# Performance work log

Hardware: AMD Instinct MI355X
Metric: run time of the kernel (lower is better)

## Reference

```python
import jax, jax.numpy as jnp
import numpy as np

IN_FEATURES = 512
OUT_FEATURES = 512
GRID_MIN = -2.0
GRID_MAX = 2.0
NUM_GRIDS = 8
SPLINE_SCALE = 0.1
BATCH = 16384


def setup_inputs() -> dict:
    key = jax.random.key(0)
    kx, kw = jax.random.split(key)
    x = jax.random.normal(kx, (BATCH, IN_FEATURES), dtype=jnp.float32)
    grid = jnp.linspace(GRID_MIN, GRID_MAX, NUM_GRIDS, dtype=jnp.float32)
    spline_weight = (
        jax.random.normal(kw, (IN_FEATURES * NUM_GRIDS, OUT_FEATURES), dtype=jnp.float32)
        * SPLINE_SCALE
    )
    return {"x": x, "grid": grid, "spline_weight": spline_weight}


def reference(x, grid, spline_weight):
    # denominator h = (grid_max - grid_min) / (num_grids - 1)
    h = (GRID_MAX - GRID_MIN) / (NUM_GRIDS - 1)
    # basis: [B, in_features, num_grids]
    basis = jnp.exp(-jnp.square((x[..., None] - grid) / h))
    # flatten to [B, in_features * num_grids] and GEMM
    return basis.reshape(basis.shape[0], -1) @ spline_weight
```

## Files before the change

### kernel.cpp

```cpp
#include <hip/hip_runtime.h>
#include <hip/hip_bf16.h>

#define BATCH 16384
#define IN_F 512
#define OUT_F 512
#define NG 8
#define KTOT (IN_F * NG)

#define SH    2.1019642153762872f
#define SSTEP 1.2011224087864498f
#define BC0N  4.2039284307525745f
#define RC1   2.4022448175728996f

typedef __attribute__((ext_vector_type(8))) short short8;
typedef __attribute__((ext_vector_type(4))) float f32x4;
typedef __attribute__((ext_vector_type(2))) float f32x2;
typedef __attribute__((ext_vector_type(4))) unsigned int u32x4;
typedef __attribute__((ext_vector_type(2))) unsigned int u32x2;

__device__ __forceinline__ unsigned fbits(float f) {
    union { float f; unsigned u; } v; v.f = f; return v.u;
}
__device__ __forceinline__ unsigned pack2bf(float lo, float hi) {
    return __builtin_amdgcn_perm(fbits(hi) + 0x8000u, fbits(lo) + 0x8000u,
                                 0x07060302u);
}

__device__ __forceinline__ void lds_barrier() {
    __asm__ volatile("" ::: "memory");
    __builtin_amdgcn_sched_barrier(0);
    __builtin_amdgcn_s_waitcnt(0xC07F);
    __builtin_amdgcn_s_barrier();
    __builtin_amdgcn_sched_barrier(0);
    __asm__ volatile("" ::: "memory");
}

__global__ void wt_swizzle(const float* __restrict__ W, unsigned short* __restrict__ Wt) {
    const int gid  = blockIdx.x * 256 + threadIdx.x;
    const int lane = gid & 63;
    const int f    = (gid >> 6) & 7;
    const int kt   = (gid >> 9) & 63;
    const int s    = gid >> 15;
    const int j  = f & 3, kk = f >> 2;
    const int l15 = lane & 15, lq = lane >> 4;
    const int n  = s * 64 + j * 16 + l15;
    const int k0 = kt * 64 + kk * 32 + lq * 8;
    constexpr float QS[8] = {1.0f,
                             3.6787944117144233e-1f,
                             1.8315638888734179e-2f,
                             1.2340980408667956e-4f,
                             1.1253517471925912e-7f,
                             1.3887943864964021e-11f,
                             2.3195228302435693e-16f,
                             5.2428856633634640e-22f};
    u32x4 pk;
#pragma unroll
    for (int e = 0; e < 4; ++e)
        pk[e] = pack2bf(W[(size_t)(k0 + 2 * e) * OUT_F + n] * QS[2 * e],
                        W[(size_t)(k0 + 2 * e + 1) * OUT_F + n] * QS[2 * e + 1]);
    *(u32x4*)(Wt + (size_t)gid * 8) = pk;
}

__global__ __launch_bounds__(512, 2) void gauss_gemm18(
        const float* __restrict__ X, const unsigned short* __restrict__ Wt,
        float* __restrict__ Out) {
    __shared__ __align__(16) unsigned short sA[8 * 8192];

    const int tid  = threadIdx.x;
    const int lane = tid & 63;
    const int wave = tid >> 6;
    const int wm   = wave >> 2;
    const int wn   = wave & 3;
    const int nb = (blockIdx.x & 7) * 32 + (blockIdx.x >> 3);
    const int cb = nb >> 7;
    const int rb = nb & 127;
    const int m0 = rb * 128;
    const int l15 = lane & 15;
    const int lq  = lane >> 4;
    const int s   = cb * 4 + wn;

    const int arow = tid & 127;
    const int fp   = tid >> 7;
    const int aw0 = arow * 64 + (((2 * fp)     ^ (arow & 7)) << 3);
    const int aw1 = arow * 64 + (((2 * fp + 1) ^ (arow & 7)) << 3);
    const float* xlp = X + (size_t)(m0 + arow) * IN_F + fp * 2;

    int aofs[2][4];
#pragma unroll
    for (int kk = 0; kk < 2; ++kk)
#pragma unroll
        for (int i = 0; i < 4; ++i)
            aofs[kk][i] = (wm * 64 + i * 16 + l15) * 64 +
                          (((kk * 4 + lq) ^ (l15 & 7)) << 3);

    const unsigned short* bptr = Wt + (size_t)s * 262144 + lane * 8;

    f32x4 acc[4][4];
#pragma unroll
    for (int i = 0; i < 4; ++i)
#pragma unroll
        for (int j = 0; j < 4; ++j)
            acc[i][j] = (f32x4){0.f, 0.f, 0.f, 0.f};

    auto stageA = [&](f32x2 xv, int slot) {
        unsigned short* base = sA + slot * 8192;
#pragma unroll
        for (int h = 0; h < 2; ++h) {
            const float t0  = fmaf(h ? xv.y : xv.x, SH, BC0N);
            const float rho = __builtin_amdgcn_exp2f(t0 * RC1);
            const float v0  = __builtin_amdgcn_exp2f(-t0 * t0);
            const float r2  = rho * rho;
            const float v1 = v0 * rho;
            const float v2 = v0 * r2, v3 = v1 * r2;
            const float v4 = v2 * r2, v5 = v3 * r2;
            const float v6 = v4 * r2, v7 = v5 * r2;
            union { __hip_bfloat162 hh[4]; u32x4 u; } pk;
            pk.hh[0] = __float22bfloat162_rn(make_float2(v0, v1));
            pk.hh[1] = __float22bfloat162_rn(make_float2(v2, v3));
            pk.hh[2] = __float22bfloat162_rn(make_float2(v4, v5));
            pk.hh[3] = __float22bfloat162_rn(make_float2(v6, v7));
            *(u32x4*)(base + (h ? aw1 : aw0)) = pk.u;
        }
    };

    short8 bfA[8], bfB[8];
    f32x2 xu, xv;

    {
        f32x2 x0 = *(const f32x2*)(xlp);
        f32x2 x1 = *(const f32x2*)(xlp + 8);
        f32x2 x2 = *(const f32x2*)(xlp + 16);
        f32x2 x3 = *(const f32x2*)(xlp + 24);
        xu = *(const f32x2*)(xlp + 32);
        xv = *(const f32x2*)(xlp + 40);
#pragma unroll
        for (int f = 0; f < 8; ++f)
            bfA[f] = *(const short8*)(bptr + f * 512);
        stageA(x0, 0);
        stageA(x1, 1);
        stageA(x2, 2);
        stageA(x3, 3);
        lds_barrier();
    }

#define GG18(KT0, S, BU, BF, XUSE)                                             \
    {                                                                          \
        const int kt  = (KT0) + (S);                                           \
        const int kn1 = (kt + 1 < 64) ? kt + 1 : 63;                           \
        const int kn6 = (kt + 6 < 64) ? kt + 6 : 63;                           \
        _Pragma("unroll")                                                      \
        for (int f = 0; f < 8; ++f)                                            \
            BF[f] = *(const short8*)(bptr + (size_t)kn1 * 4096 + f * 512);     \
        short8 af[2][4];                                                       \
        _Pragma("unroll")                                                      \
        for (int kk = 0; kk < 2; ++kk)                                         \
            _Pragma("unroll")                                                  \
            for (int i = 0; i < 4; ++i)                                        \
                af[kk][i] = *(const short8*)(sA + (S) * 8192 + aofs[kk][i]);   \
        stageA(XUSE, ((S) + 4) & 7);                                           \
        XUSE = *(const f32x2*)(xlp + (size_t)kn6 * 8);                         \
        __builtin_amdgcn_s_setprio(1);                                         \
        _Pragma("unroll")                                                      \
        for (int kk = 0; kk < 2; ++kk)                                         \
            _Pragma("unroll")                                                  \
            for (int i = 0; i < 4; ++i)                                        \
                _Pragma("unroll")                                              \
                for (int j = 0; j < 4; ++j)                                    \
                    acc[i][j] = __builtin_amdgcn_mfma_f32_16x16x32_bf16(       \
                        af[kk][i], BU[kk * 4 + j], acc[i][j], 0, 0, 0);        \
        __builtin_amdgcn_s_setprio(0);                                         \
        if (((S) & 3) == 3) lds_barrier();                                     \
    }

    for (int kt0 = 0; kt0 < 64; kt0 += 8) {
        GG18(kt0, 0, bfA, bfB, xu)
        GG18(kt0, 1, bfB, bfA, xv)
        GG18(kt0, 2, bfA, bfB, xu)
        GG18(kt0, 3, bfB, bfA, xv)
        GG18(kt0, 4, bfA, bfB, xu)
        GG18(kt0, 5, bfB, bfA, xv)
        GG18(kt0, 6, bfA, bfB, xu)
        GG18(kt0, 7, bfB, bfA, xv)
    }
#undef GG18

#pragma unroll
    for (int i = 0; i < 4; ++i) {
        const int r0 = m0 + wm * 64 + i * 16 + lq * 4;
#pragma unroll
        for (int j = 0; j < 4; ++j) {
            const int c = cb * 256 + wn * 64 + j * 16 + l15;
#pragma unroll
            for (int e = 0; e < 4; ++e)
                Out[(size_t)(r0 + e) * OUT_F + c] = acc[i][j][e];
        }
    }
}

#define BM 128
#define BN 128
#define BK 64
#define LDA 72
#define LDB 72

__global__ __launch_bounds__(256, 2) void gauss_gemm_fb(
        const float* __restrict__ X, const float* __restrict__ W,
        float* __restrict__ Out) {
    __shared__ __align__(16) unsigned short sA[BM * LDA];
    __shared__ __align__(16) unsigned short sB2[BN * LDB];

    const int tid  = threadIdx.x;
    const int lane = tid & 63;
    const int wave = tid >> 6;
    const int rb = blockIdx.x >> 2;
    const int cbx = blockIdx.x & 3;
    const int m0 = rb * BM;
    const int n0 = cbx * BN;
    const int wr = (wave >> 1) * 64;
    const int wc = (wave & 1) * 64;
    const int l15 = lane & 15;
    const int lq  = lane >> 4;

    f32x4 acc[4][4];
#pragma unroll
    for (int i = 0; i < 4; ++i)
#pragma unroll
        for (int j = 0; j < 4; ++j)
            acc[i][j] = (f32x4){0.f, 0.f, 0.f, 0.f};

    const int arow = tid & 127;
    const int axq  = tid >> 7;

    for (int kt = 0; kt < KTOT / BK; ++kt) {
        const int k0  = kt * BK;
        const int xc0 = kt * (BK / NG);

        const f32x4 xv = *(const f32x4*)(X + (size_t)(m0 + arow) * IN_F + xc0 + 4 * axq);
        unsigned short* sArow = sA + arow * LDA + axq * 32;
#pragma unroll
        for (int j = 0; j < 4; ++j) {
            const float xs = xv[j] * SH;
            u32x4 pk;
#pragma unroll
            for (int g = 0; g < 8; g += 2) {
                float t0 = xs + (BC0N - g * SSTEP);
                float t1 = xs + (BC0N - (g + 1) * SSTEP);
                pk[g >> 1] = pack2bf(__builtin_amdgcn_exp2f(-t0 * t0),
                                     __builtin_amdgcn_exp2f(-t1 * t1));
            }
            *(u32x4*)(sArow + j * 8) = pk;
        }

#pragma unroll
        for (int p = 0; p < 8; ++p) {
            int id = p * 256 + tid;
            int n  = id & 127;
            int k4 = id >> 7;
            const float* wp = W + (size_t)(k0 + k4 * 4) * OUT_F + n0 + n;
            u32x2 v;
            v[0] = pack2bf(wp[0], wp[OUT_F]);
            v[1] = pack2bf(wp[2 * OUT_F], wp[3 * OUT_F]);
            *(u32x2*)(sB2 + n * LDB + k4 * 4) = v;
        }

        __syncthreads();

#pragma unroll
        for (int kk = 0; kk < BK; kk += 32) {
            short8 af[4], bfv[4];
#pragma unroll
            for (int i = 0; i < 4; ++i)
                af[i] = *(const short8*)(sA + (wr + i * 16 + l15) * LDA + kk + lq * 8);
#pragma unroll
            for (int i = 0; i < 4; ++i)
                bfv[i] = *(const short8*)(sB2 + (wc + i * 16 + l15) * LDB + kk + lq * 8);
#pragma unroll
            for (int i = 0; i < 4; ++i)
#pragma unroll
                for (int j = 0; j < 4; ++j)
                    acc[i][j] = __builtin_amdgcn_mfma_f32_16x16x32_bf16(af[i], bfv[j], acc[i][j], 0, 0, 0);
        }

        __syncthreads();
    }

#pragma unroll
    for (int i = 0; i < 4; ++i) {
        const int r0 = m0 + wr + i * 16 + lq * 4;
#pragma unroll
        for (int j = 0; j < 4; ++j) {
            const int c = n0 + wc + j * 16 + l15;
#pragma unroll
            for (int e = 0; e < 4; ++e)
                Out[(size_t)(r0 + e) * OUT_F + c] = acc[i][j][e];
        }
    }
}

extern "C" void kernel_launch(void* const* d_in, const int* in_sizes, int n_in,
                              void* d_out, int out_size, void* d_ws, size_t ws_size,
                              hipStream_t stream) {
    (void)in_sizes; (void)n_in; (void)out_size;
    const float* X = (const float*)d_in[0];
    const float* W = (const float*)d_in[2];
    float* Out = (float*)d_out;

    const size_t wt_bytes = (size_t)KTOT * OUT_F * sizeof(unsigned short);
    if (ws_size >= wt_bytes) {
        unsigned short* Wt = (unsigned short*)d_ws;
        wt_swizzle<<<dim3(KTOT * OUT_F / 8 / 256), 256, 0, stream>>>(W, Wt);
        gauss_gemm18<<<dim3((BATCH / 128) * (OUT_F / 256)), 512, 0, stream>>>(X, Wt, Out);
    } else {
        gauss_gemm_fb<<<dim3((BATCH / BM) * (OUT_F / BN)), 256, 0, stream>>>(X, W, Out);
    }
}
```

Before: 154.7 us.

## Split waves into producer (basis compute) and consumer (MFMA) roles

```diff
diff --git a/kernel.cpp b/kernel.cpp
--- a/kernel.cpp
+++ b/kernel.cpp
@@ -61,93 +61,50 @@
     *(u32x4*)(Wt + (size_t)gid * 8) = pk;
 }
 
-__global__ __launch_bounds__(512, 2) void gauss_gemm18(
+__global__ __launch_bounds__(512, 2) void gauss_gemm20(
         const float* __restrict__ X, const unsigned short* __restrict__ Wt,
         float* __restrict__ Out) {
-    __shared__ __align__(16) unsigned short sA[8 * 8192];
+    __shared__ __align__(16) unsigned short sA[8 * 4096];
 
     const int tid  = threadIdx.x;
     const int lane = tid & 63;
     const int wave = tid >> 6;
-    const int wm   = wave >> 2;
-    const int wn   = wave & 3;
-    const int nb = (blockIdx.x & 7) * 32 + (blockIdx.x >> 3);
-    const int cb = nb >> 7;
-    const int rb = nb & 127;
-    const int m0 = rb * 128;
+    const int nb = (blockIdx.x & 7) * 64 + (blockIdx.x >> 3);
+    const int cb = nb >> 8;
+    const int rb = nb & 255;
+    const int m0 = rb * 64;
     const int l15 = lane & 15;
     const int lq  = lane >> 4;
-    const int s   = cb * 4 + wn;
-
-    const int arow = tid & 127;
-    const int fp   = tid >> 7;
-    const int aw0 = arow * 64 + (((2 * fp)     ^ (arow & 7)) << 3);
-    const int aw1 = arow * 64 + (((2 * fp + 1) ^ (arow & 7)) << 3);
-    const float* xlp = X + (size_t)(m0 + arow) * IN_F + fp * 2;
-
-    int aofs[2][4];
-#pragma unroll
-    for (int kk = 0; kk < 2; ++kk)
+
+    if (wave < 4) {
+        const int s = cb * 4 + wave;
+        const unsigned short* bptr = Wt + (size_t)s * 262144 + lane * 8;
+
+        int aofs[2][4];
+#pragma unroll
+        for (int kk = 0; kk < 2; ++kk)
+#pragma unroll
+            for (int i = 0; i < 4; ++i)
+                aofs[kk][i] = (i * 16 + l15) * 64 +
+                              (((kk * 4 + lq) ^ (l15 & 7)) << 3);
+
+        f32x4 acc[4][4];
 #pragma unroll
         for (int i = 0; i < 4; ++i)
-            aofs[kk][i] = (wm * 64 + i * 16 + l15) * 64 +
-                          (((kk * 4 + lq) ^ (l15 & 7)) << 3);
-
-    const unsigned short* bptr = Wt + (size_t)s * 262144 + lane * 8;
-
-    f32x4 acc[4][4];
-#pragma unroll
-    for (int i = 0; i < 4; ++i)
-#pragma unroll
-        for (int j = 0; j < 4; ++j)
-            acc[i][j] = (f32x4){0.f, 0.f, 0.f, 0.f};
-
-    auto stageA = [&](f32x2 xv, int slot) {
-        unsigned short* base = sA + slot * 8192;
-#pragma unroll
-        for (int h = 0; h < 2; ++h) {
-            const float t0  = fmaf(h ? xv.y : xv.x, SH, BC0N);
-            const float rho = __builtin_amdgcn_exp2f(t0 * RC1);
-            const float v0  = __builtin_amdgcn_exp2f(-t0 * t0);
-            const float r2  = rho * rho;
-            const float v1 = v0 * rho;
-            const float v2 = v0 * r2, v3 = v1 * r2;
-            const float v4 = v2 * r2, v5 = v3 * r2;
-            const float v6 = v4 * r2, v7 = v5 * r2;
-            union { __hip_bfloat162 hh[4]; u32x4 u; } pk;
-            pk.hh[0] = __float22bfloat162_rn(make_float2(v0, v1));
-            pk.hh[1] = __float22bfloat162_rn(make_float2(v2, v3));
-            pk.hh[2] = __float22bfloat162_rn(make_float2(v4, v5));
-            pk.hh[3] = __float22bfloat162_rn(make_float2(v6, v7));
-            *(u32x4*)(base + (h ? aw1 : aw0)) = pk.u;
-        }
-    };
-
-    short8 bfA[8], bfB[8];
-    f32x2 xu, xv;
-
-    {
-        f32x2 x0 = *(const f32x2*)(xlp);
-        f32x2 x1 = *(const f32x2*)(xlp + 8);
-        f32x2 x2 = *(const f32x2*)(xlp + 16);
-        f32x2 x3 = *(const f32x2*)(xlp + 24);
-        xu = *(const f32x2*)(xlp + 32);
-        xv = *(const f32x2*)(xlp + 40);
+#pragma unroll
+            for (int j = 0; j < 4; ++j)
+                acc[i][j] = (f32x4){0.f, 0.f, 0.f, 0.f};
+
+        short8 bfA[8], bfB[8];
 #pragma unroll
         for (int f = 0; f < 8; ++f)
             bfA[f] = *(const short8*)(bptr + f * 512);
-        stageA(x0, 0);
-        stageA(x1, 1);
-        stageA(x2, 2);
-        stageA(x3, 3);
+
         lds_barrier();
-    }
-
-#define GG18(KT0, S, BU, BF, XUSE)                                             \
+
+#define CONS20(KT, BU, BF)                                                     \
     {                                                                          \
-        const int kt  = (KT0) + (S);                                           \
-        const int kn1 = (kt + 1 < 64) ? kt + 1 : 63;                           \
-        const int kn6 = (kt + 6 < 64) ? kt + 6 : 63;                           \
+        const int kn1 = ((KT) + 1 < 64) ? (KT) + 1 : 63;                       \
         _Pragma("unroll")                                                      \
         for (int f = 0; f < 8; ++f)                                            \
             BF[f] = *(const short8*)(bptr + (size_t)kn1 * 4096 + f * 512);     \
@@ -156,9 +113,8 @@
         for (int kk = 0; kk < 2; ++kk)                                         \
             _Pragma("unroll")                                                  \
             for (int i = 0; i < 4; ++i)                                        \
-                af[kk][i] = *(const short8*)(sA + (S) * 8192 + aofs[kk][i]);   \
-        stageA(XUSE, ((S) + 4) & 7);                                           \
-        XUSE = *(const f32x2*)(xlp + (size_t)kn6 * 8);                         \
+                af[kk][i] = *(const short8*)(sA + ((KT) & 7) * 4096 +          \
+                                             aofs[kk][i]);                     \
         __builtin_amdgcn_s_setprio(1);                                         \
         _Pragma("unroll")                                                      \
         for (int kk = 0; kk < 2; ++kk)                                         \
@@ -169,30 +125,112 @@
                     acc[i][j] = __builtin_amdgcn_mfma_f32_16x16x32_bf16(       \
                         af[kk][i], BU[kk * 4 + j], acc[i][j], 0, 0, 0);        \
         __builtin_amdgcn_s_setprio(0);                                         \
-        if (((S) & 3) == 3) lds_barrier();                                     \
-    }
-
-    for (int kt0 = 0; kt0 < 64; kt0 += 8) {
-        GG18(kt0, 0, bfA, bfB, xu)
-        GG18(kt0, 1, bfB, bfA, xv)
-        GG18(kt0, 2, bfA, bfB, xu)
-        GG18(kt0, 3, bfB, bfA, xv)
-        GG18(kt0, 4, bfA, bfB, xu)
-        GG18(kt0, 5, bfB, bfA, xv)
-        GG18(kt0, 6, bfA, bfB, xu)
-        GG18(kt0, 7, bfB, bfA, xv)
-    }
-#undef GG18
-
-#pragma unroll
-    for (int i = 0; i < 4; ++i) {
-        const int r0 = m0 + wm * 64 + i * 16 + lq * 4;
-#pragma unroll
-        for (int j = 0; j < 4; ++j) {
-            const int c = cb * 256 + wn * 64 + j * 16 + l15;
-#pragma unroll
-            for (int e = 0; e < 4; ++e)
-                Out[(size_t)(r0 + e) * OUT_F + c] = acc[i][j][e];
+    }
+
+        for (int kt0 = 0; kt0 < 64; kt0 += 8) {
+            CONS20(kt0 + 0, bfA, bfB)
+            CONS20(kt0 + 1, bfB, bfA)
+            CONS20(kt0 + 2, bfA, bfB)
+            CONS20(kt0 + 3, bfB, bfA)
+            lds_barrier();
+            CONS20(kt0 + 4, bfA, bfB)
+            CONS20(kt0 + 5, bfB, bfA)
+            CONS20(kt0 + 6, bfA, bfB)
+            CONS20(kt0 + 7, bfB, bfA)
+            lds_barrier();
+        }
+#undef CONS20
+
+#pragma unroll
+        for (int i = 0; i < 4; ++i) {
+            const int r0 = m0 + i * 16 + lq * 4;
+#pragma unroll
+            for (int j = 0; j < 4; ++j) {
+                const int c = cb * 256 + wave * 64 + j * 16 + l15;
+#pragma unroll
+                for (int e = 0; e < 4; ++e)
+                    Out[(size_t)(r0 + e) * OUT_F + c] = acc[i][j][e];
+            }
+        }
+    } else {
+        const int pid = wave - 4;
+        const int aw0 = lane * 64 + (((2 * pid)     ^ (lane & 7)) << 3);
+        const int aw1 = lane * 64 + (((2 * pid + 1) ^ (lane & 7)) << 3);
+        const float* xlp = X + (size_t)(m0 + lane) * IN_F + pid * 2;
+
+        auto stageA = [&](f32x2 xv, int slot) {
+            unsigned short* base = sA + slot * 4096;
+#pragma unroll
+            for (int h = 0; h < 2; ++h) {
+                const float t0  = fmaf(h ? xv.y : xv.x, SH, BC0N);
+                const float rho = __builtin_amdgcn_exp2f(t0 * RC1);
+                const float v0  = __builtin_amdgcn_exp2f(-t0 * t0);
+                const float r2  = rho * rho;
+                const float v1 = v0 * rho;
+                const float v2 = v0 * r2, v3 = v1 * r2;
+                const float v4 = v2 * r2, v5 = v3 * r2;
+                const float v6 = v4 * r2, v7 = v5 * r2;
+                union { __hip_bfloat162 hh[4]; u32x4 u; } pk;
+                pk.hh[0] = __float22bfloat162_rn(make_float2(v0, v1));
+                pk.hh[1] = __float22bfloat162_rn(make_float2(v2, v3));
+                pk.hh[2] = __float22bfloat162_rn(make_float2(v4, v5));
+                pk.hh[3] = __float22bfloat162_rn(make_float2(v6, v7));
+                *(u32x4*)(base + (h ? aw1 : aw0)) = pk.u;
+            }
+        };
+
+        {
+            f32x2 t0 = *(const f32x2*)(xlp);
+            f32x2 t1 = *(const f32x2*)(xlp + 8);
+            f32x2 t2 = *(const f32x2*)(xlp + 16);
+            f32x2 t3 = *(const f32x2*)(xlp + 24);
+            stageA(t0, 0);
+            stageA(t1, 1);
+            stageA(t2, 2);
+            stageA(t3, 3);
+        }
+        f32x2 xA0 = *(const f32x2*)(xlp + 32);
+        f32x2 xA1 = *(const f32x2*)(xlp + 40);
+        f32x2 xA2 = *(const f32x2*)(xlp + 48);
+        f32x2 xA3 = *(const f32x2*)(xlp + 56);
+        f32x2 xB0 = *(const f32x2*)(xlp + 64);
+        f32x2 xB1 = *(const f32x2*)(xlp + 72);
+        f32x2 xB2 = *(const f32x2*)(xlp + 80);
+        f32x2 xB3 = *(const f32x2*)(xlp + 88);
+
+        lds_barrier();
+
+        for (int kt0 = 0; kt0 < 64; kt0 += 8) {
+            stageA(xA0, (kt0 + 4) & 7);
+            stageA(xA1, (kt0 + 5) & 7);
+            stageA(xA2, (kt0 + 6) & 7);
+            stageA(xA3, (kt0 + 7) & 7);
+            {
+                const int ka = (kt0 + 12 < 64) ? kt0 + 12 : 63;
+                const int kb = (kt0 + 13 < 64) ? kt0 + 13 : 63;
+                const int kc = (kt0 + 14 < 64) ? kt0 + 14 : 63;
+                const int kd = (kt0 + 15 < 64) ? kt0 + 15 : 63;
+                xA0 = *(const f32x2*)(xlp + (size_t)ka * 8);
+                xA1 = *(const f32x2*)(xlp + (size_t)kb * 8);
+                xA2 = *(const f32x2*)(xlp + (size_t)kc * 8);
+                xA3 = *(const f32x2*)(xlp + (size_t)kd * 8);
+            }
+            lds_barrier();
+            if (kt0 < 56) {
+                stageA(xB0, (kt0 + 8) & 7);
+                stageA(xB1, (kt0 + 9) & 7);
+                stageA(xB2, (kt0 + 10) & 7);
+                stageA(xB3, (kt0 + 11) & 7);
+                const int ka = (kt0 + 16 < 64) ? kt0 + 16 : 63;
+                const int kb = (kt0 + 17 < 64) ? kt0 + 17 : 63;
+                const int kc = (kt0 + 18 < 64) ? kt0 + 18 : 63;
+                const int kd = (kt0 + 19 < 64) ? kt0 + 19 : 63;
+                xB0 = *(const f32x2*)(xlp + (size_t)ka * 8);
+                xB1 = *(const f32x2*)(xlp + (size_t)kb * 8);
+                xB2 = *(const f32x2*)(xlp + (size_t)kc * 8);
+                xB3 = *(const f32x2*)(xlp + (size_t)kd * 8);
+            }
+            lds_barrier();
         }
     }
 }
@@ -309,7 +347,7 @@
     if (ws_size >= wt_bytes) {
         unsigned short* Wt = (unsigned short*)d_ws;
         wt_swizzle<<<dim3(KTOT * OUT_F / 8 / 256), 256, 0, stream>>>(W, Wt);
-        gauss_gemm18<<<dim3((BATCH / 128) * (OUT_F / 256)), 512, 0, stream>>>(X, Wt, Out);
+        gauss_gemm20<<<dim3((BATCH / 64) * (OUT_F / 256)), 512, 0, stream>>>(X, Wt, Out);
     } else {
         gauss_gemm_fb<<<dim3((BATCH / BM) * (OUT_F / BN)), 256, 0, stream>>>(X, W, Out);
     }
```

After: 154.7 us. No clear change (+0.0%).
